# Performance work log

Hardware: AMD Instinct MI355X
Metric: run time of the kernel (lower is better)

Reference implementation:

```python
import jax, jax.numpy as jnp
import numpy as np

N_WAY, K_SHOT = 5, 1
N_CLASSES = 64
D = 8


def _conv(x, w, b):
    y = jax.lax.conv_general_dilated(x, w, (2, 2), 'SAME',
                                     dimension_numbers=('NCHW', 'OIHW', 'NCHW'))
    return jax.nn.relu(y + b[None, :, None, None])


def setup_inputs() -> dict:
    key = jax.random.key(0)
    ks = jax.random.split(key, 12)
    b, s_sup, q, h, w = 4, N_WAY * K_SHOT, 1, 64, 64
    rnd = lambda k, shape: jax.random.normal(k, shape, jnp.float32) * 0.05
    return {
        'support_x': jax.random.normal(ks[0], (b, s_sup, 3, h, w), jnp.float32),
        'support_y': jax.random.randint(ks[1], (b, s_sup), 0, N_CLASSES),
        'query_x': jax.random.normal(ks[2], (b, q, 3, h, w), jnp.float32),
        'query_y': jax.random.randint(ks[3], (b, q), 0, N_CLASSES),
        'k1': rnd(ks[4], (32, 3, 3, 3)), 'bc1': jnp.zeros((32,), jnp.float32),
        'k2': rnd(ks[5], (48, 32, 3, 3)), 'bc2': jnp.zeros((48,), jnp.float32),
        'k3': rnd(ks[6], (64, 48, 3, 3)), 'bc3': jnp.zeros((64,), jnp.float32),
        'Wlog': rnd(ks[7], (64, N_CLASSES)), 'blog': jnp.zeros((N_CLASSES,), jnp.float32),
        'Wg1': rnd(ks[8], (132, 128)), 'bg1': jnp.zeros((128,), jnp.float32),
        'Wg2': rnd(ks[9], (128, 64)), 'bg2': jnp.zeros((64,), jnp.float32),
        'Wf1': rnd(ks[10], (64, 16)), 'bf1': jnp.zeros((16,), jnp.float32),
        'Wf2': rnd(ks[11], (16, 1)), 'bf2': jnp.zeros((1,), jnp.float32),
    }


def reference(support_x, support_y, query_x, query_y,
              k1, bc1, k2, bc2, k3, bc3, Wlog, blog,
              Wg1, bg1, Wg2, bg2, Wf1, bf1, Wf2, bf2):
    x = jnp.concatenate([support_x, query_x], axis=1)       # [b, s, 3, h, w]
    label = jnp.concatenate([support_y, query_y], axis=1)   # [b, s]
    b, s = label.shape
    h, w = x.shape[-2:]

    feat = x.reshape(b * s, 3, h, w)
    feat = _conv(feat, k1, bc1)
    feat = _conv(feat, k2, bc2)
    feat = _conv(feat, k3, bc3)                              # [b*s, c, D, D]
    c = feat.shape[1]
    logits = feat.mean(axis=(2, 3)) @ Wlog + blog            # [b*s, n_classes]

    # --- append normalized (i/d, j/d) coord channels ---
    ii = jnp.arange(D, dtype=feat.dtype) / D
    coord = jnp.stack([jnp.broadcast_to(ii[:, None], (D, D)),
                       jnp.broadcast_to(ii[None, :], (D, D))])        # [2, D, D]
    feat = feat.reshape(b, s, c, D, D)
    feat = jnp.concatenate([feat, jnp.broadcast_to(coord, (b, s, 2, D, D))], axis=2)
    c2 = c + 2
    m = D * D
    a = feat.reshape(b, s, c2, m).transpose(0, 1, 3, 2)      # [b, s, m, c2]

    # --- relation network g over all (set-pair, position-pair) combos ---
    # original: g(concat(x_i, x_j)) where x_i = x[b, j, :, q], x_j = x[b, i, :, p]
    # split first linear: concat @ Wg1 = x_i @ Wg1[:c2] + x_j @ Wg1[c2:]
    W1a, W1b = Wg1[:c2], Wg1[c2:]
    u = a @ W1a                                              # [b, s_j, m_q, 128]
    v = a @ W1b + bg1                                        # [b, s_i, m_p, 128]
    # hdd[b,i,j,q,p] = relu(u[b,j,q] + v[b,i,p])  -> [b, s, s, m, m, 128]
    hdd = jax.nn.relu(u[:, None, :, :, None, :] + v[:, :, None, None, :, :])
    g = jax.nn.relu(hdd @ Wg2 + bg2)                         # [b, s, s, m, m, 64]
    x_f = g.sum(axis=(3, 4))                                 # [b, s, s, 64]
    score = jax.nn.sigmoid(jax.nn.relu(x_f @ Wf1 + bf1) @ Wf2 + bf2)  # [b, s, s, 1]

    # --- losses ---
    logp = jax.nn.log_softmax(logits, axis=-1)
    lab = label.reshape(-1)
    cls_loss = -jnp.take_along_axis(logp, lab[:, None], axis=1).mean()

    y = (label[:, :, None] == label[:, None, :])[..., None].astype(score.dtype)
    P = score[..., 0]                                        # [b, s, s]
    Pt = P.transpose(0, 2, 1)
    sym, anti = 0.5 * (P + Pt), 0.5 * (P - Pt)
    sym_n = jnp.sqrt((sym ** 2).sum(axis=(1, 2)))            # Frobenius per batch
    anti_n = jnp.sqrt((anti ** 2).sum(axis=(1, 2)))
    sym_loss = ((sym_n - anti_n) / (sym_n + anti_n)).mean()
    euc_loss = ((score - y) ** 2).mean()
    rn_loss = euc_loss - 0.1 * sym_loss
    return (cls_loss, rn_loss, sym_loss)
```

## Files before the change

### kernel.cpp

```cpp
#include <hip/hip_runtime.h>

typedef _Float16 f16x8 __attribute__((ext_vector_type(8)));
typedef float f32x4 __attribute__((ext_vector_type(4)));

__global__ void conv1_k(const float* __restrict__ sx, const float* __restrict__ qx,
                        const float* __restrict__ w, const float* __restrict__ bias,
                        float* __restrict__ out,
                        const float* __restrict__ Wg2, _Float16* __restrict__ W2h) {
    if (blockIdx.x == 768) {
        for (int s = 0; s < 4; s++) {
            int slot = threadIdx.x + 256*s;
            int tile = slot >> 6, lane = slot & 63;
            int kt = tile >> 2, nt = tile & 3;
            int quad = lane >> 4, col = lane & 15;
            f16x8 t;
            #pragma unroll
            for (int jj = 0; jj < 8; jj++)
                t[jj] = (_Float16)Wg2[(kt*32 + quad*8 + jj)*64 + nt*16 + col];
            *(f16x8*)&W2h[slot*8] = t;
        }
        return;
    }
    int n  = blockIdx.x >> 5;
    int oc = blockIdx.x & 31;
    int bi = n / 6, si = n % 6;
    const float* inp = (si < 5) ? sx + (size_t)((bi*5+si)*3)*4096
                                : qx + (size_t)(bi*3)*4096;
    __shared__ float wl[27];
    __shared__ float bl;
    if (threadIdx.x < 27) wl[threadIdx.x] = w[oc*27 + threadIdx.x];
    if (threadIdx.x == 0) bl = bias[oc];
    __syncthreads();
    for (int idx = threadIdx.x; idx < 1024; idx += 256) {
        int oy = idx >> 5, ox = idx & 31;
        float acc = bl;
        #pragma unroll
        for (int ic = 0; ic < 3; ic++) {
            const float* ip = inp + ic*4096;
            #pragma unroll
            for (int dy = 0; dy < 3; dy++) {
                int iy = 2*oy + dy;
                if (iy >= 64) continue;
                #pragma unroll
                for (int dx = 0; dx < 3; dx++) {
                    int ix = 2*ox + dx;
                    if (ix >= 64) continue;
                    acc += ip[iy*64+ix] * wl[ic*9 + dy*3 + dx];
                }
            }
        }
        out[(size_t)(n*32+oc)*1024 + idx] = fmaxf(acc, 0.f);
    }
}

__global__ void conv2_k(const float* __restrict__ in, const float* __restrict__ w,
                        const float* __restrict__ bias, float* __restrict__ out) {
    int n   = blockIdx.x / 12;
    int ocg = blockIdx.x % 12;
    __shared__ float wl[4*32*9];
    for (int e = threadIdx.x; e < 1152; e += 256) wl[e] = w[ocg*4*288 + e];
    __syncthreads();
    int oy = threadIdx.x >> 4, ox = threadIdx.x & 15;
    float a0 = bias[ocg*4+0], a1 = bias[ocg*4+1], a2 = bias[ocg*4+2], a3 = bias[ocg*4+3];
    const float* ib = in + (size_t)n*32*1024;
    for (int ic = 0; ic < 32; ic++) {
        const float* ip = ib + ic*1024;
        float tap[9];
        #pragma unroll
        for (int dy = 0; dy < 3; dy++)
            #pragma unroll
            for (int dx = 0; dx < 3; dx++) {
                int iy = 2*oy+dy, ix = 2*ox+dx;
                tap[dy*3+dx] = (iy < 32 && ix < 32) ? ip[iy*32+ix] : 0.f;
            }
        #pragma unroll
        for (int t = 0; t < 9; t++) {
            a0 += tap[t]*wl[0*288 + ic*9 + t];
            a1 += tap[t]*wl[1*288 + ic*9 + t];
            a2 += tap[t]*wl[2*288 + ic*9 + t];
            a3 += tap[t]*wl[3*288 + ic*9 + t];
        }
    }
    size_t ob = (size_t)(n*48 + ocg*4)*256 + threadIdx.x;
    out[ob        ] = fmaxf(a0, 0.f);
    out[ob + 256  ] = fmaxf(a1, 0.f);
    out[ob + 512  ] = fmaxf(a2, 0.f);
    out[ob + 768  ] = fmaxf(a3, 0.f);
}

__global__ void conv3_k(const float* __restrict__ in, const float* __restrict__ w,
                        const float* __restrict__ bias, float* __restrict__ out,
                        float* __restrict__ mf) {
    int n   = blockIdx.x >> 3;
    int ocg = blockIdx.x & 7;
    __shared__ float wl[8*48*9];
    for (int e = threadIdx.x; e < 3456; e += 256) wl[e] = w[ocg*8*432 + e];
    __syncthreads();
    int pix = threadIdx.x & 63, osub = threadIdx.x >> 6;
    int oy = pix >> 3, ox = pix & 7;
    int ol0 = osub*2;
    float a0 = bias[ocg*8 + ol0], a1 = bias[ocg*8 + ol0 + 1];
    const float* ib = in + (size_t)n*48*256;
    for (int ic = 0; ic < 48; ic++) {
        const float* ip = ib + ic*256;
        float tap[9];
        #pragma unroll
        for (int dy = 0; dy < 3; dy++)
            #pragma unroll
            for (int dx = 0; dx < 3; dx++) {
                int iy = 2*oy+dy, ix = 2*ox+dx;
                tap[dy*3+dx] = (iy < 16 && ix < 16) ? ip[iy*16+ix] : 0.f;
            }
        #pragma unroll
        for (int t = 0; t < 9; t++) {
            a0 += tap[t]*wl[ ol0   *432 + ic*9 + t];
            a1 += tap[t]*wl[(ol0+1)*432 + ic*9 + t];
        }
    }
    float r0 = fmaxf(a0, 0.f), r1 = fmaxf(a1, 0.f);
    out[(size_t)(n*64 + ocg*8 + ol0  )*64 + pix] = r0;
    out[(size_t)(n*64 + ocg*8 + ol0+1)*64 + pix] = r1;
    #pragma unroll
    for (int off = 32; off >= 1; off >>= 1) {
        r0 += __shfl_xor(r0, off, 64);
        r1 += __shfl_xor(r1, off, 64);
    }
    if (pix == 0) {
        mf[n*64 + ocg*8 + ol0    ] = r0 * (1.f/64.f);
        mf[n*64 + ocg*8 + ol0 + 1] = r1 * (1.f/64.f);
    }
}

__global__ void uvcls_k(const float* __restrict__ feat3, const float* __restrict__ Wg1,
                        const float* __restrict__ bg1, _Float16* __restrict__ u,
                        _Float16* __restrict__ v,
                        const float* __restrict__ mf, const int* __restrict__ sy,
                        const int* __restrict__ qy, const float* __restrict__ Wlog,
                        const float* __restrict__ blog, float* __restrict__ rv) {
    int tid = threadIdx.x;
    if (blockIdx.x >= 384) {
        int n = blockIdx.x - 384;
        if (tid >= 64) return;
        int lane = tid;
        float s = blog[lane];
        for (int c = 0; c < 64; c++) s += mf[n*64 + c] * Wlog[c*64 + lane];
        float mx = s;
        #pragma unroll
        for (int off = 32; off >= 1; off >>= 1) mx = fmaxf(mx, __shfl_xor(mx, off, 64));
        float p = __expf(s - mx);
        float se = p;
        #pragma unroll
        for (int off = 32; off >= 1; off >>= 1) se += __shfl_xor(se, off, 64);
        int bi = n/6, si = n%6;
        int lab = (si < 5) ? sy[bi*5+si] : qy[bi];
        float s_lab = __shfl(s, lab, 64);
        if (lane == 0) rv[n] = -(s_lab - mx - __logf(se));
        return;
    }
    int bs = blockIdx.x >> 4;
    int pg = blockIdx.x & 15;
    __shared__ float a4[4][66];
    for (int e = tid; e < 264; e += 128) {
        int pl = e / 66, c = e % 66;
        int p = pg*4 + pl;
        float vv;
        if (c < 64)       vv = feat3[(size_t)(bs*64 + c)*64 + p];
        else if (c == 64) vv = (float)(p >> 3) * 0.125f;
        else              vv = (float)(p & 7) * 0.125f;
        a4[pl][c] = vv;
    }
    __syncthreads();
    float us[4] = {0.f,0.f,0.f,0.f};
    float bg = bg1[tid];
    float vs[4] = {bg,bg,bg,bg};
    for (int c = 0; c < 66; c++) {
        float wa = Wg1[c*128 + tid];
        float wb = Wg1[(66+c)*128 + tid];
        #pragma unroll
        for (int pl = 0; pl < 4; pl++) {
            us[pl] += a4[pl][c]*wa;
            vs[pl] += a4[pl][c]*wb;
        }
    }
    #pragma unroll
    for (int pl = 0; pl < 4; pl++) {
        int p = pg*4 + pl;
        u[(size_t)(bs*64+p)*128 + tid] = (_Float16)us[pl];
        v[(size_t)(bs*64+p)*128 + tid] = (_Float16)vs[pl];
    }
}

__global__ void __launch_bounds__(256) rel_k(
        const _Float16* __restrict__ U, const _Float16* __restrict__ V,
        const _Float16* __restrict__ W2h, const float* __restrict__ bg2,
        float* __restrict__ xfpart) {
    __shared__ __align__(16) _Float16 Vsh[16*128];
    __shared__ float xfred[4][64];

    int bx = blockIdx.x;
    int cb = bx >> 2, qc = bx & 3;
    int b = cb / 36, rem = cb % 36;
    int j = rem / 6, i = rem % 6;
    int tid  = threadIdx.x;
    int wv   = tid >> 6, lane = tid & 63;
    int col  = lane & 15, quad = lane >> 4;

    const _Float16* ub = U + (size_t)(b*6 + i)*8192;
    const _Float16* vb = V + (size_t)(b*6 + j)*8192 + qc*16*128;

    *(f16x8*)&Vsh[tid*8] = *(const f16x8*)&vb[tid*8];

    f16x8 uf[4];
    {
        const _Float16* up = ub + (wv*16 + col)*128 + quad*8;
        #pragma unroll
        for (int kt = 0; kt < 4; kt++) uf[kt] = *(const f16x8*)&up[kt*32];
    }
    f16x8 bf[4][4];
    #pragma unroll
    for (int kt = 0; kt < 4; kt++)
        #pragma unroll
        for (int nt = 0; nt < 4; nt++)
            bf[kt][nt] = *(const f16x8*)&W2h[(size_t)(((kt*4+nt)*64) + lane)*8];
    float bgv[4];
    #pragma unroll
    for (int nt = 0; nt < 4; nt++) bgv[nt] = bg2[nt*16 + col];

    __syncthreads();

    float sums[4] = {0.f,0.f,0.f,0.f};
    for (int q = 0; q < 16; q++) {
        const _Float16* vp = &Vsh[q*128 + quad*8];
        f32x4 acc[4];
        #pragma unroll
        for (int nt = 0; nt < 4; nt++)
            acc[nt] = (f32x4){bgv[nt], bgv[nt], bgv[nt], bgv[nt]};
        #pragma unroll
        for (int kt = 0; kt < 4; kt++) {
            f16x8 vf = *(const f16x8*)&vp[kt*32];
            f16x8 af = uf[kt] + vf;
            af = __builtin_elementwise_max(af, (f16x8){0,0,0,0,0,0,0,0});
            #pragma unroll
            for (int nt = 0; nt < 4; nt++)
                acc[nt] = __builtin_amdgcn_mfma_f32_16x16x32_f16(af, bf[kt][nt], acc[nt], 0, 0, 0);
        }
        #pragma unroll
        for (int nt = 0; nt < 4; nt++)
            #pragma unroll
            for (int rr = 0; rr < 4; rr++)
                sums[nt] += fmaxf(acc[nt][rr], 0.f);
    }

    #pragma unroll
    for (int nt = 0; nt < 4; nt++) {
        sums[nt] += __shfl_xor(sums[nt], 16, 64);
        sums[nt] += __shfl_xor(sums[nt], 32, 64);
    }
    if (lane < 16) {
        #pragma unroll
        for (int nt = 0; nt < 4; nt++) xfred[wv][nt*16 + lane] = sums[nt];
    }
    __syncthreads();
    if (tid < 64)
        xfpart[(size_t)bx*64 + tid] = xfred[0][tid] + xfred[1][tid] + xfred[2][tid] + xfred[3][tid];
}

__global__ void loss_k(const float* __restrict__ xfp, const float* __restrict__ rv,
                       const int* __restrict__ sy, const int* __restrict__ qy,
                       const float* __restrict__ Wf1, const float* __restrict__ bf1,
                       const float* __restrict__ Wf2, const float* __restrict__ bf2,
                       float* __restrict__ out) {
    __shared__ float Wf1sh[1024];
    __shared__ float wf2sh[16];
    __shared__ float bf1sh[16];
    __shared__ float Pm[144];
    __shared__ int lab[24];
    __shared__ float red[256];
    __shared__ float ratio[4];
    int tid = threadIdx.x;
    for (int e = tid; e < 1024; e += 256) Wf1sh[e] = Wf1[e];
    if (tid < 16) { wf2sh[tid] = Wf2[tid]; bf1sh[tid] = bf1[tid]; }
    if (tid < 24) { int bi = tid/6, si = tid%6; lab[tid] = (si < 5) ? sy[bi*5+si] : qy[bi]; }
    __syncthreads();
    if (tid < 144) {
        float hid[16];
        #pragma unroll
        for (int h = 0; h < 16; h++) hid[h] = bf1sh[h];
        const float* xb = xfp + (size_t)tid*4*64;
        for (int n = 0; n < 64; n++) {
            float x = xb[n] + xb[64+n] + xb[128+n] + xb[192+n];
            #pragma unroll
            for (int h = 0; h < 16; h++) hid[h] += x * Wf1sh[n*16 + h];
        }
        float sc = bf2[0];
        #pragma unroll
        for (int h = 0; h < 16; h++) sc += fmaxf(hid[h], 0.f) * wf2sh[h];
        Pm[tid] = 1.f/(1.f + __expf(-sc));
    }
    __syncthreads();
    float e = 0.f;
    if (tid < 144) {
        int b = tid/36, r = tid%36, jj = r/6, ii = r%6;
        float y = (lab[b*6+jj] == lab[b*6+ii]) ? 1.f : 0.f;
        float d = Pm[tid] - y;
        e = d*d;
    }
    red[tid] = e;
    __syncthreads();
    for (int s = 128; s > 0; s >>= 1) {
        if (tid < s) red[tid] += red[tid+s];
        __syncthreads();
    }
    if (tid < 4) {
        float s2 = 0.f, a2 = 0.f;
        for (int jj = 0; jj < 6; jj++)
            for (int ii = 0; ii < 6; ii++) {
                float pa = Pm[tid*36 + jj*6 + ii], pb = Pm[tid*36 + ii*6 + jj];
                float sm = 0.5f*(pa+pb), an = 0.5f*(pa-pb);
                s2 += sm*sm; a2 += an*an;
            }
        float sn = sqrtf(s2), anq = sqrtf(a2);
        ratio[tid] = (sn - anq)/(sn + anq);
    }
    __syncthreads();
    if (tid == 0) {
        float sl = 0.25f*(ratio[0]+ratio[1]+ratio[2]+ratio[3]);
        float euc = red[0] * (1.f/144.f);
        float cs = 0.f;
        for (int k = 0; k < 24; k++) cs += rv[k];
        out[0] = cs * (1.f/24.f);
        out[1] = euc - 0.1f*sl;
        out[2] = sl;
    }
}

extern "C" void kernel_launch(void* const* d_in, const int* in_sizes, int n_in,
                              void* d_out, int out_size, void* d_ws, size_t ws_size,
                              hipStream_t stream) {
    const float* sx   = (const float*)d_in[0];
    const int*   sy   = (const int*)  d_in[1];
    const float* qx   = (const float*)d_in[2];
    const int*   qy   = (const int*)  d_in[3];
    const float* k1   = (const float*)d_in[4];
    const float* bc1  = (const float*)d_in[5];
    const float* k2   = (const float*)d_in[6];
    const float* bc2  = (const float*)d_in[7];
    const float* k3   = (const float*)d_in[8];
    const float* bc3  = (const float*)d_in[9];
    const float* Wlog = (const float*)d_in[10];
    const float* blog = (const float*)d_in[11];
    const float* Wg1  = (const float*)d_in[12];
    const float* bg1  = (const float*)d_in[13];
    const float* Wg2  = (const float*)d_in[14];
    const float* bg2  = (const float*)d_in[15];
    const float* Wf1  = (const float*)d_in[16];
    const float* bf1  = (const float*)d_in[17];
    const float* Wf2  = (const float*)d_in[18];
    const float* bf2  = (const float*)d_in[19];

    float* ws    = (float*)d_ws;
    float* feat1 = ws;
    float* feat2 = feat1 + 786432;
    float* feat3 = feat2 + 294912;
    float* mf    = feat3 + 98304;
    float* rv    = mf    + 1536;
    float* xfp   = rv    + 32;
    _Float16* u16 = (_Float16*)(xfp + 36864);
    _Float16* v16 = u16 + 196608;
    _Float16* W2h = v16 + 196608;
    float* out   = (float*)d_out;

    conv1_k <<<769,    256, 0, stream>>>(sx, qx, k1, bc1, feat1, Wg2, W2h);
    conv2_k <<<24*12,  256, 0, stream>>>(feat1, k2, bc2, feat2);
    conv3_k <<<24*8,   256, 0, stream>>>(feat2, k3, bc3, feat3, mf);
    uvcls_k <<<408,    128, 0, stream>>>(feat3, Wg1, bg1, u16, v16,
                                         mf, sy, qy, Wlog, blog, rv);
    rel_k   <<<576,    256, 0, stream>>>(u16, v16, W2h, bg2, xfp);
    loss_k  <<<1,      256, 0, stream>>>(xfp, rv, sy, qy, Wf1, bf1, Wf2, bf2, out);
}
```

Measured before the change: 189.7 us.

## Fuse all stages into one persistent kernel with software grid barriers

Replaces the six separate kernel launches with one persistent mega-kernel sized to occupancy. Stages are separated by an atomic-counter global barrier, and blocks loop over each stage's work chunks. The goal is to remove per-launch overhead and the idle gaps between stages. The uv projection now packs two pixel groups per 256-thread block, and the relation partial sums are stored transposed so the loss stage can read them as vector loads. The barrier depends on every block being resident at once. The counter is never reset but grows monotonically across calls, which may eventually risk wraparound.

```diff
diff --git a/kernel.cpp b/kernel.cpp
--- a/kernel.cpp
+++ b/kernel.cpp
@@ -3,378 +3,395 @@
 typedef _Float16 f16x8 __attribute__((ext_vector_type(8)));
 typedef float f32x4 __attribute__((ext_vector_type(4)));
 
-__global__ void conv1_k(const float* __restrict__ sx, const float* __restrict__ qx,
-                        const float* __restrict__ w, const float* __restrict__ bias,
-                        float* __restrict__ out,
-                        const float* __restrict__ Wg2, _Float16* __restrict__ W2h) {
-    if (blockIdx.x == 768) {
-        for (int s = 0; s < 4; s++) {
-            int slot = threadIdx.x + 256*s;
-            int tile = slot >> 6, lane = slot & 63;
-            int kt = tile >> 2, nt = tile & 3;
-            int quad = lane >> 4, col = lane & 15;
-            f16x8 t;
-            #pragma unroll
-            for (int jj = 0; jj < 8; jj++)
-                t[jj] = (_Float16)Wg2[(kt*32 + quad*8 + jj)*64 + nt*16 + col];
-            *(f16x8*)&W2h[slot*8] = t;
-        }
-        return;
-    }
-    int n  = blockIdx.x >> 5;
-    int oc = blockIdx.x & 31;
-    int bi = n / 6, si = n % 6;
-    const float* inp = (si < 5) ? sx + (size_t)((bi*5+si)*3)*4096
-                                : qx + (size_t)(bi*3)*4096;
-    __shared__ float wl[27];
-    __shared__ float bl;
-    if (threadIdx.x < 27) wl[threadIdx.x] = w[oc*27 + threadIdx.x];
-    if (threadIdx.x == 0) bl = bias[oc];
+__device__ unsigned g_bar_count = 0;
+
+struct MegaP {
+    const float* sx; const int* sy; const float* qx; const int* qy;
+    const float* k1; const float* bc1; const float* k2; const float* bc2;
+    const float* k3; const float* bc3; const float* Wlog; const float* blog;
+    const float* Wg1; const float* bg1; const float* Wg2; const float* bg2;
+    const float* Wf1; const float* bf1; const float* Wf2; const float* bf2;
+    float* feat1; float* feat2; float* feat3; float* mf; float* rv; float* xfpT;
+    _Float16* u16; _Float16* v16; _Float16* W2h; float* out;
+};
+
+__device__ __forceinline__ void gbar() {
     __syncthreads();
-    for (int idx = threadIdx.x; idx < 1024; idx += 256) {
-        int oy = idx >> 5, ox = idx & 31;
-        float acc = bl;
+    if (threadIdx.x == 0) {
+        __threadfence();
+        unsigned nb = gridDim.x;
+        unsigned my = __hip_atomic_fetch_add(&g_bar_count, 1u, __ATOMIC_ACQ_REL,
+                                             __HIP_MEMORY_SCOPE_AGENT) + 1u;
+        unsigned tgt = ((my + nb - 1u) / nb) * nb;
+        while (__hip_atomic_load(&g_bar_count, __ATOMIC_ACQUIRE,
+                                 __HIP_MEMORY_SCOPE_AGENT) < tgt)
+            __builtin_amdgcn_s_sleep(2);
+    }
+    __syncthreads();
+    __threadfence();
+}
+
+__global__ void __launch_bounds__(256, 2) mega_k(MegaP P) {
+    __shared__ __align__(16) float smem[3456];
+    const int tid = threadIdx.x;
+    const unsigned gsz = gridDim.x;
+
+    for (unsigned ch = blockIdx.x; ch < 769; ch += gsz) {
+        if (ch == 768) {
+            for (int s = 0; s < 4; s++) {
+                int slot = tid + 256*s;
+                int tile = slot >> 6, lane = slot & 63;
+                int kt = tile >> 2, nt = tile & 3;
+                int quad = lane >> 4, col = lane & 15;
+                f16x8 t;
+                #pragma unroll
+                for (int jj = 0; jj < 8; jj++)
+                    t[jj] = (_Float16)P.Wg2[(kt*32 + quad*8 + jj)*64 + nt*16 + col];
+                *(f16x8*)&P.W2h[slot*8] = t;
+            }
+        } else {
+            int n  = (int)ch >> 5;
+            int oc = (int)ch & 31;
+            int bi = n / 6, si = n % 6;
+            const float* inp = (si < 5) ? P.sx + (size_t)((bi*5+si)*3)*4096
+                                        : P.qx + (size_t)(bi*3)*4096;
+            __syncthreads();
+            if (tid < 27) smem[tid] = P.k1[oc*27 + tid];
+            if (tid == 31) smem[27] = P.bc1[oc];
+            __syncthreads();
+            float bl = smem[27];
+            for (int idx = tid; idx < 1024; idx += 256) {
+                int oy = idx >> 5, ox = idx & 31;
+                float acc = bl;
+                #pragma unroll
+                for (int ic = 0; ic < 3; ic++) {
+                    const float* ip = inp + ic*4096;
+                    #pragma unroll
+                    for (int dy = 0; dy < 3; dy++) {
+                        int iy = 2*oy + dy;
+                        if (iy >= 64) continue;
+                        #pragma unroll
+                        for (int dx = 0; dx < 3; dx++) {
+                            int ix = 2*ox + dx;
+                            if (ix >= 64) continue;
+                            acc += ip[iy*64+ix] * smem[ic*9 + dy*3 + dx];
+                        }
+                    }
+                }
+                P.feat1[(size_t)(n*32+oc)*1024 + idx] = fmaxf(acc, 0.f);
+            }
+        }
+    }
+    gbar();
+
+    for (unsigned ch = blockIdx.x; ch < 288; ch += gsz) {
+        int n   = (int)ch / 12;
+        int ocg = (int)ch % 12;
+        __syncthreads();
+        for (int e = tid; e < 1152; e += 256) smem[e] = P.k2[ocg*1152 + e];
+        __syncthreads();
+        int oy = tid >> 4, ox = tid & 15;
+        float a0 = P.bc2[ocg*4+0], a1 = P.bc2[ocg*4+1];
+        float a2 = P.bc2[ocg*4+2], a3 = P.bc2[ocg*4+3];
+        const float* ib = P.feat1 + (size_t)n*32*1024;
+        for (int ic = 0; ic < 32; ic++) {
+            const float* ip = ib + ic*1024;
+            float tap[9];
+            #pragma unroll
+            for (int dy = 0; dy < 3; dy++)
+                #pragma unroll
+                for (int dx = 0; dx < 3; dx++) {
+                    int iy = 2*oy+dy, ix = 2*ox+dx;
+                    tap[dy*3+dx] = (iy < 32 && ix < 32) ? ip[iy*32+ix] : 0.f;
+                }
+            #pragma unroll
+            for (int t = 0; t < 9; t++) {
+                a0 += tap[t]*smem[0*288 + ic*9 + t];
+                a1 += tap[t]*smem[1*288 + ic*9 + t];
+                a2 += tap[t]*smem[2*288 + ic*9 + t];
+                a3 += tap[t]*smem[3*288 + ic*9 + t];
+            }
+        }
+        size_t ob = (size_t)(n*48 + ocg*4)*256 + tid;
+        P.feat2[ob        ] = fmaxf(a0, 0.f);
+        P.feat2[ob + 256  ] = fmaxf(a1, 0.f);
+        P.feat2[ob + 512  ] = fmaxf(a2, 0.f);
+        P.feat2[ob + 768  ] = fmaxf(a3, 0.f);
+    }
+    gbar();
+
+    for (unsigned ch = blockIdx.x; ch < 192; ch += gsz) {
+        int n   = (int)ch >> 3;
+        int ocg = (int)ch & 7;
+        __syncthreads();
+        for (int e = tid; e < 3456; e += 256) smem[e] = P.k3[ocg*3456 + e];
+        __syncthreads();
+        int pix = tid & 63, osub = tid >> 6;
+        int oy = pix >> 3, ox = pix & 7;
+        int ol0 = osub*2;
+        float a0 = P.bc3[ocg*8 + ol0], a1 = P.bc3[ocg*8 + ol0 + 1];
+        const float* ib = P.feat2 + (size_t)n*48*256;
+        for (int ic = 0; ic < 48; ic++) {
+            const float* ip = ib + ic*256;
+            float tap[9];
+            #pragma unroll
+            for (int dy = 0; dy < 3; dy++)
+                #pragma unroll
+                for (int dx = 0; dx < 3; dx++) {
+                    int iy = 2*oy+dy, ix = 2*ox+dx;
+                    tap[dy*3+dx] = (iy < 16 && ix < 16) ? ip[iy*16+ix] : 0.f;
+                }
+            #pragma unroll
+            for (int t = 0; t < 9; t++) {
+                a0 += tap[t]*smem[ ol0   *432 + ic*9 + t];
+                a1 += tap[t]*smem[(ol0+1)*432 + ic*9 + t];
+            }
+        }
+        float r0 = fmaxf(a0, 0.f), r1 = fmaxf(a1, 0.f);
+        P.feat3[(size_t)(n*64 + ocg*8 + ol0  )*64 + pix] = r0;
+        P.feat3[(size_t)(n*64 + ocg*8 + ol0+1)*64 + pix] = r1;
         #pragma unroll
-        for (int ic = 0; ic < 3; ic++) {
-            const float* ip = inp + ic*4096;
-            #pragma unroll
-            for (int dy = 0; dy < 3; dy++) {
-                int iy = 2*oy + dy;
-                if (iy >= 64) continue;
-                #pragma unroll
-                for (int dx = 0; dx < 3; dx++) {
-                    int ix = 2*ox + dx;
-                    if (ix >= 64) continue;
-                    acc += ip[iy*64+ix] * wl[ic*9 + dy*3 + dx];
-                }
-            }
-        }
-        out[(size_t)(n*32+oc)*1024 + idx] = fmaxf(acc, 0.f);
-    }
-}
-
-__global__ void conv2_k(const float* __restrict__ in, const float* __restrict__ w,
-                        const float* __restrict__ bias, float* __restrict__ out) {
-    int n   = blockIdx.x / 12;
-    int ocg = blockIdx.x % 12;
-    __shared__ float wl[4*32*9];
-    for (int e = threadIdx.x; e < 1152; e += 256) wl[e] = w[ocg*4*288 + e];
-    __syncthreads();
-    int oy = threadIdx.x >> 4, ox = threadIdx.x & 15;
-    float a0 = bias[ocg*4+0], a1 = bias[ocg*4+1], a2 = bias[ocg*4+2], a3 = bias[ocg*4+3];
-    const float* ib = in + (size_t)n*32*1024;
-    for (int ic = 0; ic < 32; ic++) {
-        const float* ip = ib + ic*1024;
-        float tap[9];
+        for (int off = 32; off >= 1; off >>= 1) {
+            r0 += __shfl_xor(r0, off, 64);
+            r1 += __shfl_xor(r1, off, 64);
+        }
+        if (pix == 0) {
+            P.mf[n*64 + ocg*8 + ol0    ] = r0 * (1.f/64.f);
+            P.mf[n*64 + ocg*8 + ol0 + 1] = r1 * (1.f/64.f);
+        }
+    }
+    gbar();
+
+    for (unsigned ch = blockIdx.x; ch < 216; ch += gsz) {
+        if (ch < 192) {
+            int bs = (int)ch >> 3, pp = (int)ch & 7;
+            int half = tid >> 7, t = tid & 127;
+            int pg = pp*2 + half;
+            float (*a4)[66] = ((float(*)[66])smem) + half*4;
+            __syncthreads();
+            for (int e = t; e < 264; e += 128) {
+                int pl = e / 66, c = e % 66;
+                int p = pg*4 + pl;
+                float vv;
+                if (c < 64)       vv = P.feat3[(size_t)(bs*64 + c)*64 + p];
+                else if (c == 64) vv = (float)(p >> 3) * 0.125f;
+                else              vv = (float)(p & 7) * 0.125f;
+                a4[pl][c] = vv;
+            }
+            __syncthreads();
+            float us[4] = {0.f,0.f,0.f,0.f};
+            float bg = P.bg1[t];
+            float vs[4] = {bg,bg,bg,bg};
+            for (int c = 0; c < 66; c++) {
+                float wa = P.Wg1[c*128 + t];
+                float wb = P.Wg1[(66+c)*128 + t];
+                #pragma unroll
+                for (int pl = 0; pl < 4; pl++) {
+                    us[pl] += a4[pl][c]*wa;
+                    vs[pl] += a4[pl][c]*wb;
+                }
+            }
+            #pragma unroll
+            for (int pl = 0; pl < 4; pl++) {
+                int p = pg*4 + pl;
+                P.u16[(size_t)(bs*64+p)*128 + t] = (_Float16)us[pl];
+                P.v16[(size_t)(bs*64+p)*128 + t] = (_Float16)vs[pl];
+            }
+        } else {
+            int n = (int)ch - 192;
+            if (tid < 64) {
+                float s = P.blog[tid];
+                for (int c = 0; c < 64; c++) s += P.mf[n*64 + c] * P.Wlog[c*64 + tid];
+                float mx = s;
+                #pragma unroll
+                for (int off = 32; off >= 1; off >>= 1) mx = fmaxf(mx, __shfl_xor(mx, off, 64));
+                float px = __expf(s - mx);
+                float se = px;
+                #pragma unroll
+                for (int off = 32; off >= 1; off >>= 1) se += __shfl_xor(se, off, 64);
+                int bi = n/6, si = n%6;
+                int lab = (si < 5) ? P.sy[bi*5+si] : P.qy[bi];
+                float s_lab = __shfl(s, lab, 64);
+                if (tid == 0) P.rv[n] = -(s_lab - mx - __logf(se));
+            }
+        }
+    }
+    gbar();
+
+    {
+        int wv = tid >> 6, lane = tid & 63;
+        int col = lane & 15, quad = lane >> 4;
+        f16x8 bf[4][4];
         #pragma unroll
-        for (int dy = 0; dy < 3; dy++)
-            #pragma unroll
-            for (int dx = 0; dx < 3; dx++) {
-                int iy = 2*oy+dy, ix = 2*ox+dx;
-                tap[dy*3+dx] = (iy < 32 && ix < 32) ? ip[iy*32+ix] : 0.f;
-            }
+        for (int kt = 0; kt < 4; kt++)
+            #pragma unroll
+            for (int nt = 0; nt < 4; nt++)
+                bf[kt][nt] = *(const f16x8*)&P.W2h[(size_t)(((kt*4+nt)*64) + lane)*8];
+        float bgv[4];
         #pragma unroll
-        for (int t = 0; t < 9; t++) {
-            a0 += tap[t]*wl[0*288 + ic*9 + t];
-            a1 += tap[t]*wl[1*288 + ic*9 + t];
-            a2 += tap[t]*wl[2*288 + ic*9 + t];
-            a3 += tap[t]*wl[3*288 + ic*9 + t];
-        }
-    }
-    size_t ob = (size_t)(n*48 + ocg*4)*256 + threadIdx.x;
-    out[ob        ] = fmaxf(a0, 0.f);
-    out[ob + 256  ] = fmaxf(a1, 0.f);
-    out[ob + 512  ] = fmaxf(a2, 0.f);
-    out[ob + 768  ] = fmaxf(a3, 0.f);
-}
-
-__global__ void conv3_k(const float* __restrict__ in, const float* __restrict__ w,
-                        const float* __restrict__ bias, float* __restrict__ out,
-                        float* __restrict__ mf) {
-    int n   = blockIdx.x >> 3;
-    int ocg = blockIdx.x & 7;
-    __shared__ float wl[8*48*9];
-    for (int e = threadIdx.x; e < 3456; e += 256) wl[e] = w[ocg*8*432 + e];
-    __syncthreads();
-    int pix = threadIdx.x & 63, osub = threadIdx.x >> 6;
-    int oy = pix >> 3, ox = pix & 7;
-    int ol0 = osub*2;
-    float a0 = bias[ocg*8 + ol0], a1 = bias[ocg*8 + ol0 + 1];
-    const float* ib = in + (size_t)n*48*256;
-    for (int ic = 0; ic < 48; ic++) {
-        const float* ip = ib + ic*256;
-        float tap[9];
-        #pragma unroll
-        for (int dy = 0; dy < 3; dy++)
-            #pragma unroll
-            for (int dx = 0; dx < 3; dx++) {
-                int iy = 2*oy+dy, ix = 2*ox+dx;
-                tap[dy*3+dx] = (iy < 16 && ix < 16) ? ip[iy*16+ix] : 0.f;
-            }
-        #pragma unroll
-        for (int t = 0; t < 9; t++) {
-            a0 += tap[t]*wl[ ol0   *432 + ic*9 + t];
-            a1 += tap[t]*wl[(ol0+1)*432 + ic*9 + t];
-        }
-    }
-    float r0 = fmaxf(a0, 0.f), r1 = fmaxf(a1, 0.f);
-    out[(size_t)(n*64 + ocg*8 + ol0  )*64 + pix] = r0;
-    out[(size_t)(n*64 + ocg*8 + ol0+1)*64 + pix] = r1;
-    #pragma unroll
-    for (int off = 32; off >= 1; off >>= 1) {
-        r0 += __shfl_xor(r0, off, 64);
-        r1 += __shfl_xor(r1, off, 64);
-    }
-    if (pix == 0) {
-        mf[n*64 + ocg*8 + ol0    ] = r0 * (1.f/64.f);
-        mf[n*64 + ocg*8 + ol0 + 1] = r1 * (1.f/64.f);
-    }
-}
-
-__global__ void uvcls_k(const float* __restrict__ feat3, const float* __restrict__ Wg1,
-                        const float* __restrict__ bg1, _Float16* __restrict__ u,
-                        _Float16* __restrict__ v,
-                        const float* __restrict__ mf, const int* __restrict__ sy,
-                        const int* __restrict__ qy, const float* __restrict__ Wlog,
-                        const float* __restrict__ blog, float* __restrict__ rv) {
-    int tid = threadIdx.x;
-    if (blockIdx.x >= 384) {
-        int n = blockIdx.x - 384;
-        if (tid >= 64) return;
-        int lane = tid;
-        float s = blog[lane];
-        for (int c = 0; c < 64; c++) s += mf[n*64 + c] * Wlog[c*64 + lane];
-        float mx = s;
-        #pragma unroll
-        for (int off = 32; off >= 1; off >>= 1) mx = fmaxf(mx, __shfl_xor(mx, off, 64));
-        float p = __expf(s - mx);
-        float se = p;
-        #pragma unroll
-        for (int off = 32; off >= 1; off >>= 1) se += __shfl_xor(se, off, 64);
-        int bi = n/6, si = n%6;
-        int lab = (si < 5) ? sy[bi*5+si] : qy[bi];
-        float s_lab = __shfl(s, lab, 64);
-        if (lane == 0) rv[n] = -(s_lab - mx - __logf(se));
-        return;
-    }
-    int bs = blockIdx.x >> 4;
-    int pg = blockIdx.x & 15;
-    __shared__ float a4[4][66];
-    for (int e = tid; e < 264; e += 128) {
-        int pl = e / 66, c = e % 66;
-        int p = pg*4 + pl;
-        float vv;
-        if (c < 64)       vv = feat3[(size_t)(bs*64 + c)*64 + p];
-        else if (c == 64) vv = (float)(p >> 3) * 0.125f;
-        else              vv = (float)(p & 7) * 0.125f;
-        a4[pl][c] = vv;
-    }
-    __syncthreads();
-    float us[4] = {0.f,0.f,0.f,0.f};
-    float bg = bg1[tid];
-    float vs[4] = {bg,bg,bg,bg};
-    for (int c = 0; c < 66; c++) {
-        float wa = Wg1[c*128 + tid];
-        float wb = Wg1[(66+c)*128 + tid];
-        #pragma unroll
-        for (int pl = 0; pl < 4; pl++) {
-            us[pl] += a4[pl][c]*wa;
-            vs[pl] += a4[pl][c]*wb;
-        }
-    }
-    #pragma unroll
-    for (int pl = 0; pl < 4; pl++) {
-        int p = pg*4 + pl;
-        u[(size_t)(bs*64+p)*128 + tid] = (_Float16)us[pl];
-        v[(size_t)(bs*64+p)*128 + tid] = (_Float16)vs[pl];
-    }
-}
-
-__global__ void __launch_bounds__(256) rel_k(
-        const _Float16* __restrict__ U, const _Float16* __restrict__ V,
-        const _Float16* __restrict__ W2h, const float* __restrict__ bg2,
-        float* __restrict__ xfpart) {
-    __shared__ __align__(16) _Float16 Vsh[16*128];
-    __shared__ float xfred[4][64];
-
-    int bx = blockIdx.x;
-    int cb = bx >> 2, qc = bx & 3;
-    int b = cb / 36, rem = cb % 36;
-    int j = rem / 6, i = rem % 6;
-    int tid  = threadIdx.x;
-    int wv   = tid >> 6, lane = tid & 63;
-    int col  = lane & 15, quad = lane >> 4;
-
-    const _Float16* ub = U + (size_t)(b*6 + i)*8192;
-    const _Float16* vb = V + (size_t)(b*6 + j)*8192 + qc*16*128;
-
-    *(f16x8*)&Vsh[tid*8] = *(const f16x8*)&vb[tid*8];
-
-    f16x8 uf[4];
-    {
-        const _Float16* up = ub + (wv*16 + col)*128 + quad*8;
-        #pragma unroll
-        for (int kt = 0; kt < 4; kt++) uf[kt] = *(const f16x8*)&up[kt*32];
-    }
-    f16x8 bf[4][4];
-    #pragma unroll
-    for (int kt = 0; kt < 4; kt++)
-        #pragma unroll
-        for (int nt = 0; nt < 4; nt++)
-            bf[kt][nt] = *(const f16x8*)&W2h[(size_t)(((kt*4+nt)*64) + lane)*8];
-    float bgv[4];
-    #pragma unroll
-    for (int nt = 0; nt < 4; nt++) bgv[nt] = bg2[nt*16 + col];
-
-    __syncthreads();
-
-    float sums[4] = {0.f,0.f,0.f,0.f};
-    for (int q = 0; q < 16; q++) {
-        const _Float16* vp = &Vsh[q*128 + quad*8];
-        f32x4 acc[4];
-        #pragma unroll
-        for (int nt = 0; nt < 4; nt++)
-            acc[nt] = (f32x4){bgv[nt], bgv[nt], bgv[nt], bgv[nt]};
-        #pragma unroll
-        for (int kt = 0; kt < 4; kt++) {
-            f16x8 vf = *(const f16x8*)&vp[kt*32];
-            f16x8 af = uf[kt] + vf;
-            af = __builtin_elementwise_max(af, (f16x8){0,0,0,0,0,0,0,0});
-            #pragma unroll
-            for (int nt = 0; nt < 4; nt++)
-                acc[nt] = __builtin_amdgcn_mfma_f32_16x16x32_f16(af, bf[kt][nt], acc[nt], 0, 0, 0);
-        }
-        #pragma unroll
-        for (int nt = 0; nt < 4; nt++)
-            #pragma unroll
-            for (int rr = 0; rr < 4; rr++)
-                sums[nt] += fmaxf(acc[nt][rr], 0.f);
-    }
-
-    #pragma unroll
-    for (int nt = 0; nt < 4; nt++) {
-        sums[nt] += __shfl_xor(sums[nt], 16, 64);
-        sums[nt] += __shfl_xor(sums[nt], 32, 64);
-    }
-    if (lane < 16) {
-        #pragma unroll
-        for (int nt = 0; nt < 4; nt++) xfred[wv][nt*16 + lane] = sums[nt];
-    }
-    __syncthreads();
-    if (tid < 64)
-        xfpart[(size_t)bx*64 + tid] = xfred[0][tid] + xfred[1][tid] + xfred[2][tid] + xfred[3][tid];
-}
-
-__global__ void loss_k(const float* __restrict__ xfp, const float* __restrict__ rv,
-                       const int* __restrict__ sy, const int* __restrict__ qy,
-                       const float* __restrict__ Wf1, const float* __restrict__ bf1,
-                       const float* __restrict__ Wf2, const float* __restrict__ bf2,
-                       float* __restrict__ out) {
-    __shared__ float Wf1sh[1024];
-    __shared__ float wf2sh[16];
-    __shared__ float bf1sh[16];
-    __shared__ float Pm[144];
-    __shared__ int lab[24];
-    __shared__ float red[256];
-    __shared__ float ratio[4];
-    int tid = threadIdx.x;
-    for (int e = tid; e < 1024; e += 256) Wf1sh[e] = Wf1[e];
-    if (tid < 16) { wf2sh[tid] = Wf2[tid]; bf1sh[tid] = bf1[tid]; }
-    if (tid < 24) { int bi = tid/6, si = tid%6; lab[tid] = (si < 5) ? sy[bi*5+si] : qy[bi]; }
-    __syncthreads();
-    if (tid < 144) {
-        float hid[16];
-        #pragma unroll
-        for (int h = 0; h < 16; h++) hid[h] = bf1sh[h];
-        const float* xb = xfp + (size_t)tid*4*64;
-        for (int n = 0; n < 64; n++) {
-            float x = xb[n] + xb[64+n] + xb[128+n] + xb[192+n];
-            #pragma unroll
-            for (int h = 0; h < 16; h++) hid[h] += x * Wf1sh[n*16 + h];
-        }
-        float sc = bf2[0];
-        #pragma unroll
-        for (int h = 0; h < 16; h++) sc += fmaxf(hid[h], 0.f) * wf2sh[h];
-        Pm[tid] = 1.f/(1.f + __expf(-sc));
-    }
-    __syncthreads();
-    float e = 0.f;
-    if (tid < 144) {
-        int b = tid/36, r = tid%36, jj = r/6, ii = r%6;
-        float y = (lab[b*6+jj] == lab[b*6+ii]) ? 1.f : 0.f;
-        float d = Pm[tid] - y;
-        e = d*d;
-    }
-    red[tid] = e;
-    __syncthreads();
-    for (int s = 128; s > 0; s >>= 1) {
-        if (tid < s) red[tid] += red[tid+s];
-        __syncthreads();
-    }
-    if (tid < 4) {
-        float s2 = 0.f, a2 = 0.f;
-        for (int jj = 0; jj < 6; jj++)
-            for (int ii = 0; ii < 6; ii++) {
-                float pa = Pm[tid*36 + jj*6 + ii], pb = Pm[tid*36 + ii*6 + jj];
-                float sm = 0.5f*(pa+pb), an = 0.5f*(pa-pb);
-                s2 += sm*sm; a2 += an*an;
-            }
-        float sn = sqrtf(s2), anq = sqrtf(a2);
-        ratio[tid] = (sn - anq)/(sn + anq);
-    }
-    __syncthreads();
-    if (tid == 0) {
-        float sl = 0.25f*(ratio[0]+ratio[1]+ratio[2]+ratio[3]);
-        float euc = red[0] * (1.f/144.f);
-        float cs = 0.f;
-        for (int k = 0; k < 24; k++) cs += rv[k];
-        out[0] = cs * (1.f/24.f);
-        out[1] = euc - 0.1f*sl;
-        out[2] = sl;
+        for (int nt = 0; nt < 4; nt++) bgv[nt] = P.bg2[nt*16 + col];
+        _Float16* Vsh  = (_Float16*)smem;
+        float*    xfred = smem + 1024;
+
+        for (unsigned ch = blockIdx.x; ch < 576; ch += gsz) {
+            int cb = (int)ch >> 2, qc = (int)ch & 3;
+            int b = cb / 36, rem = cb % 36;
+            int j = rem / 6, i = rem % 6;
+            const _Float16* ub = P.u16 + (size_t)(b*6 + i)*8192;
+            const _Float16* vb = P.v16 + (size_t)(b*6 + j)*8192 + qc*2048;
+            __syncthreads();
+            *(f16x8*)&Vsh[tid*8] = *(const f16x8*)&vb[tid*8];
+            f16x8 uf[4];
+            {
+                const _Float16* up = ub + (wv*16 + col)*128 + quad*8;
+                #pragma unroll
+                for (int kt = 0; kt < 4; kt++) uf[kt] = *(const f16x8*)&up[kt*32];
+            }
+            __syncthreads();
+            float sums[4] = {0.f,0.f,0.f,0.f};
+            for (int q = 0; q < 16; q++) {
+                const _Float16* vp = &Vsh[q*128 + quad*8];
+                f32x4 acc[4];
+                #pragma unroll
+                for (int nt = 0; nt < 4; nt++)
+                    acc[nt] = (f32x4){bgv[nt], bgv[nt], bgv[nt], bgv[nt]};
+                #pragma unroll
+                for (int kt = 0; kt < 4; kt++) {
+                    f16x8 vf = *(const f16x8*)&vp[kt*32];
+                    f16x8 af = uf[kt] + vf;
+                    af = __builtin_elementwise_max(af, (f16x8){0,0,0,0,0,0,0,0});
+                    #pragma unroll
+                    for (int nt = 0; nt < 4; nt++)
+                        acc[nt] = __builtin_amdgcn_mfma_f32_16x16x32_f16(af, bf[kt][nt], acc[nt], 0, 0, 0);
+                }
+                #pragma unroll
+                for (int nt = 0; nt < 4; nt++)
+                    #pragma unroll
+                    for (int rr = 0; rr < 4; rr++)
+                        sums[nt] += fmaxf(acc[nt][rr], 0.f);
+            }
+            #pragma unroll
+            for (int nt = 0; nt < 4; nt++) {
+                sums[nt] += __shfl_xor(sums[nt], 16, 64);
+                sums[nt] += __shfl_xor(sums[nt], 32, 64);
+            }
+            if (lane < 16) {
+                #pragma unroll
+                for (int nt = 0; nt < 4; nt++) xfred[wv*64 + nt*16 + lane] = sums[nt];
+            }
+            __syncthreads();
+            if (tid < 64)
+                P.xfpT[(size_t)tid*576 + ch] =
+                    xfred[tid] + xfred[64+tid] + xfred[128+tid] + xfred[192+tid];
+        }
+    }
+    gbar();
+
+    if (blockIdx.x == 0) {
+        float* Wf1sh = smem;
+        float* wf2sh = smem + 1024;
+        float* bf1sh = smem + 1040;
+        float* Pmm   = smem + 1056;
+        int*   lab   = (int*)(smem + 1200);
+        float* red   = smem + 1232;
+        float* ratio = smem + 1488;
+        for (int e = tid; e < 1024; e += 256) Wf1sh[e] = P.Wf1[e];
+        if (tid < 16) { wf2sh[tid] = P.Wf2[tid]; bf1sh[tid] = P.bf1[tid]; }
+        if (tid < 24) { int bi = tid/6, si = tid%6; lab[tid] = (si < 5) ? P.sy[bi*5+si] : P.qy[bi]; }
+        __syncthreads();
+        if (tid < 144) {
+            float hid[16];
+            #pragma unroll
+            for (int h = 0; h < 16; h++) hid[h] = bf1sh[h];
+            for (int n = 0; n < 64; n++) {
+                f32x4 vv = *(const f32x4*)&P.xfpT[(size_t)n*576 + tid*4];
+                float x = vv[0] + vv[1] + vv[2] + vv[3];
+                #pragma unroll
+                for (int h = 0; h < 16; h++) hid[h] += x * Wf1sh[n*16 + h];
+            }
+            float sc = P.bf2[0];
+            #pragma unroll
+            for (int h = 0; h < 16; h++) sc += fmaxf(hid[h], 0.f) * wf2sh[h];
+            Pmm[tid] = 1.f/(1.f + __expf(-sc));
+        }
+        __syncthreads();
+        float e = 0.f;
+        if (tid < 144) {
+            int b = tid/36, r = tid%36, jj = r/6, ii = r%6;
+            float y = (lab[b*6+jj] == lab[b*6+ii]) ? 1.f : 0.f;
+            float d = Pmm[tid] - y;
+            e = d*d;
+        }
+        red[tid] = e;
+        __syncthreads();
+        for (int s = 128; s > 0; s >>= 1) {
+            if (tid < s) red[tid] += red[tid+s];
+            __syncthreads();
+        }
+        if (tid < 4) {
+            float s2 = 0.f, a2 = 0.f;
+            for (int jj = 0; jj < 6; jj++)
+                for (int ii = 0; ii < 6; ii++) {
+                    float pa = Pmm[tid*36 + jj*6 + ii], pb = Pmm[tid*36 + ii*6 + jj];
+                    float sm = 0.5f*(pa+pb), an = 0.5f*(pa-pb);
+                    s2 += sm*sm; a2 += an*an;
+                }
+            float sn = sqrtf(s2), anq = sqrtf(a2);
+            ratio[tid] = (sn - anq)/(sn + anq);
+        }
+        __syncthreads();
+        if (tid == 0) {
+            float sl = 0.25f*(ratio[0]+ratio[1]+ratio[2]+ratio[3]);
+            float euc = red[0] * (1.f/144.f);
+            float cs = 0.f;
+            for (int k = 0; k < 24; k++) cs += P.rv[k];
+            P.out[0] = cs * (1.f/24.f);
+            P.out[1] = euc - 0.1f*sl;
+            P.out[2] = sl;
+        }
     }
 }
 
 extern "C" void kernel_launch(void* const* d_in, const int* in_sizes, int n_in,
                               void* d_out, int out_size, void* d_ws, size_t ws_size,
                               hipStream_t stream) {
-    const float* sx   = (const float*)d_in[0];
-    const int*   sy   = (const int*)  d_in[1];
-    const float* qx   = (const float*)d_in[2];
-    const int*   qy   = (const int*)  d_in[3];
-    const float* k1   = (const float*)d_in[4];
-    const float* bc1  = (const float*)d_in[5];
-    const float* k2   = (const float*)d_in[6];
-    const float* bc2  = (const float*)d_in[7];
-    const float* k3   = (const float*)d_in[8];
-    const float* bc3  = (const float*)d_in[9];
-    const float* Wlog = (const float*)d_in[10];
-    const float* blog = (const float*)d_in[11];
-    const float* Wg1  = (const float*)d_in[12];
-    const float* bg1  = (const float*)d_in[13];
-    const float* Wg2  = (const float*)d_in[14];
-    const float* bg2  = (const float*)d_in[15];
-    const float* Wf1  = (const float*)d_in[16];
-    const float* bf1  = (const float*)d_in[17];
-    const float* Wf2  = (const float*)d_in[18];
-    const float* bf2  = (const float*)d_in[19];
-
     float* ws    = (float*)d_ws;
     float* feat1 = ws;
     float* feat2 = feat1 + 786432;
     float* feat3 = feat2 + 294912;
     float* mf    = feat3 + 98304;
     float* rv    = mf    + 1536;
-    float* xfp   = rv    + 32;
-    _Float16* u16 = (_Float16*)(xfp + 36864);
+    float* xfpT  = rv    + 32;
+    _Float16* u16 = (_Float16*)(xfpT + 36864);
     _Float16* v16 = u16 + 196608;
     _Float16* W2h = v16 + 196608;
-    float* out   = (float*)d_out;
-
-    conv1_k <<<769,    256, 0, stream>>>(sx, qx, k1, bc1, feat1, Wg2, W2h);
-    conv2_k <<<24*12,  256, 0, stream>>>(feat1, k2, bc2, feat2);
-    conv3_k <<<24*8,   256, 0, stream>>>(feat2, k3, bc3, feat3, mf);
-    uvcls_k <<<408,    128, 0, stream>>>(feat3, Wg1, bg1, u16, v16,
-                                         mf, sy, qy, Wlog, blog, rv);
-    rel_k   <<<576,    256, 0, stream>>>(u16, v16, W2h, bg2, xfp);
-    loss_k  <<<1,      256, 0, stream>>>(xfp, rv, sy, qy, Wf1, bf1, Wf2, bf2, out);
+
+    MegaP P;
+    P.sx = (const float*)d_in[0];  P.sy  = (const int*)d_in[1];
+    P.qx = (const float*)d_in[2];  P.qy  = (const int*)d_in[3];
+    P.k1 = (const float*)d_in[4];  P.bc1 = (const float*)d_in[5];
+    P.k2 = (const float*)d_in[6];  P.bc2 = (const float*)d_in[7];
+    P.k3 = (const float*)d_in[8];  P.bc3 = (const float*)d_in[9];
+    P.Wlog = (const float*)d_in[10]; P.blog = (const float*)d_in[11];
+    P.Wg1  = (const float*)d_in[12]; P.bg1  = (const float*)d_in[13];
+    P.Wg2  = (const float*)d_in[14]; P.bg2  = (const float*)d_in[15];
+    P.Wf1  = (const float*)d_in[16]; P.bf1  = (const float*)d_in[17];
+    P.Wf2  = (const float*)d_in[18]; P.bf2  = (const float*)d_in[19];
+    P.feat1 = feat1; P.feat2 = feat2; P.feat3 = feat3; P.mf = mf; P.rv = rv;
+    P.xfpT = xfpT; P.u16 = u16; P.v16 = v16; P.W2h = W2h; P.out = (float*)d_out;
+
+    static int grid = 0;
+    if (grid == 0) {
+        int nb = 0;
+        if (hipOccupancyMaxActiveBlocksPerMultiprocessor(&nb, mega_k, 256, 0) != hipSuccess || nb < 1)
+            nb = 1;
+        int dev = 0;
+        hipGetDevice(&dev);
+        hipDeviceProp_t prop;
+        int ncu = (hipGetDeviceProperties(&prop, dev) == hipSuccess) ? prop.multiProcessorCount : 0;
+        if (ncu < 1) ncu = 64;
+        long g = (long)nb * (long)ncu;
+        grid = (int)(g < 576 ? g : 576);
+    }
+    hipLaunchKernelGGL(mega_k, dim3(grid), dim3(256), 0, stream, P);
 }
```

Result: slower. 454.7 us (+139.7%).

## Remap block indices for XCD locality and stage conv2/conv3 inputs in LDS

Applied to the files above, without the earlier changes.

Block indices across conv1, conv2, conv3, uvcls and rel kernels are remapped so that blockIdx & 7 selects the sample or batch, aiming to place blocks that share input data on the same XCD's L2 under round-robin dispatch. conv2 and conv3 now stage each input channel plane in padded shared memory with a triple buffer and register prefetch two channels ahead, replacing strided global tap reads. This adds a __syncthreads per input channel and more LDS per block, which may reduce occupancy and add barrier cost.

```diff
diff --git a/kernel.cpp b/kernel.cpp
--- a/kernel.cpp
+++ b/kernel.cpp
@@ -2,6 +2,7 @@
 
 typedef _Float16 f16x8 __attribute__((ext_vector_type(8)));
 typedef float f32x4 __attribute__((ext_vector_type(4)));
+
 
 __global__ void conv1_k(const float* __restrict__ sx, const float* __restrict__ qx,
                         const float* __restrict__ w, const float* __restrict__ bias,
@@ -21,8 +22,9 @@
         }
         return;
     }
-    int n  = blockIdx.x >> 5;
-    int oc = blockIdx.x & 31;
+    int r8 = blockIdx.x & 7, q = blockIdx.x >> 3;
+    int n  = (q >> 5)*8 + r8;
+    int oc = q & 31;
     int bi = n / 6, si = n % 6;
     const float* inp = (si < 5) ? sx + (size_t)((bi*5+si)*3)*4096
                                 : qx + (size_t)(bi*3)*4096;
@@ -55,23 +57,36 @@
 
 __global__ void conv2_k(const float* __restrict__ in, const float* __restrict__ w,
                         const float* __restrict__ bias, float* __restrict__ out) {
-    int n   = blockIdx.x / 12;
-    int ocg = blockIdx.x % 12;
-    __shared__ float wl[4*32*9];
-    for (int e = threadIdx.x; e < 1152; e += 256) wl[e] = w[ocg*4*288 + e];
-    __syncthreads();
-    int oy = threadIdx.x >> 4, ox = threadIdx.x & 15;
-    float a0 = bias[ocg*4+0], a1 = bias[ocg*4+1], a2 = bias[ocg*4+2], a3 = bias[ocg*4+3];
+    int r8 = blockIdx.x & 7, q = blockIdx.x >> 3;
+    int n   = (q / 12)*8 + r8;
+    int ocg = q % 12;
+    __shared__ float wl[1152];
+    __shared__ float pin[3][33*32];
+    const int tid = threadIdx.x;
+    for (int e = tid; e < 1152; e += 256) wl[e] = w[ocg*1152 + e];
     const float* ib = in + (size_t)n*32*1024;
+    int srow = (tid*4) >> 5, scol = (tid*4) & 31;
+    {
+        f32x4 t0 = *(const f32x4*)&ib[tid*4];
+        float* d = &pin[0][srow*33 + scol];
+        d[0]=t0[0]; d[1]=t0[1]; d[2]=t0[2]; d[3]=t0[3];
+    }
+    f32x4 t1 = *(const f32x4*)&ib[1024 + tid*4];
+    __syncthreads();
+    int oy = tid >> 4, ox = tid & 15;
+    float a0 = bias[ocg*4+0], a1 = bias[ocg*4+1];
+    float a2 = bias[ocg*4+2], a3 = bias[ocg*4+3];
     for (int ic = 0; ic < 32; ic++) {
-        const float* ip = ib + ic*1024;
+        f32x4 t2 = t1;
+        if (ic + 2 < 32) t2 = *(const f32x4*)&ib[(size_t)(ic+2)*1024 + tid*4];
+        const float* pp = pin[ic % 3];
         float tap[9];
         #pragma unroll
         for (int dy = 0; dy < 3; dy++)
             #pragma unroll
             for (int dx = 0; dx < 3; dx++) {
                 int iy = 2*oy+dy, ix = 2*ox+dx;
-                tap[dy*3+dx] = (iy < 32 && ix < 32) ? ip[iy*32+ix] : 0.f;
+                tap[dy*3+dx] = (iy < 32 && ix < 32) ? pp[iy*33 + ix] : 0.f;
             }
         #pragma unroll
         for (int t = 0; t < 9; t++) {
@@ -80,8 +95,14 @@
             a2 += tap[t]*wl[2*288 + ic*9 + t];
             a3 += tap[t]*wl[3*288 + ic*9 + t];
         }
-    }
-    size_t ob = (size_t)(n*48 + ocg*4)*256 + threadIdx.x;
+        if (ic + 1 < 32) {
+            float* d = &pin[(ic+1) % 3][srow*33 + scol];
+            d[0]=t1[0]; d[1]=t1[1]; d[2]=t1[2]; d[3]=t1[3];
+        }
+        t1 = t2;
+        __syncthreads();
+    }
+    size_t ob = (size_t)(n*48 + ocg*4)*256 + tid;
     out[ob        ] = fmaxf(a0, 0.f);
     out[ob + 256  ] = fmaxf(a1, 0.f);
     out[ob + 512  ] = fmaxf(a2, 0.f);
@@ -91,31 +112,42 @@
 __global__ void conv3_k(const float* __restrict__ in, const float* __restrict__ w,
                         const float* __restrict__ bias, float* __restrict__ out,
                         float* __restrict__ mf) {
-    int n   = blockIdx.x >> 3;
-    int ocg = blockIdx.x & 7;
-    __shared__ float wl[8*48*9];
-    for (int e = threadIdx.x; e < 3456; e += 256) wl[e] = w[ocg*8*432 + e];
-    __syncthreads();
-    int pix = threadIdx.x & 63, osub = threadIdx.x >> 6;
+    int r8 = blockIdx.x & 7, q = blockIdx.x >> 3;
+    int n   = (q >> 3)*8 + r8;
+    int ocg = q & 7;
+    __shared__ float wl[3456];
+    __shared__ float pin[3][17*16];
+    const int tid = threadIdx.x;
+    for (int e = tid; e < 3456; e += 256) wl[e] = w[ocg*3456 + e];
+    const float* ib = in + (size_t)n*48*256;
+    int srow = tid >> 4, scol = tid & 15;
+    pin[0][srow*17 + scol] = ib[tid];
+    float t1 = ib[256 + tid];
+    __syncthreads();
+    int pix = tid & 63, osub = tid >> 6;
     int oy = pix >> 3, ox = pix & 7;
     int ol0 = osub*2;
     float a0 = bias[ocg*8 + ol0], a1 = bias[ocg*8 + ol0 + 1];
-    const float* ib = in + (size_t)n*48*256;
     for (int ic = 0; ic < 48; ic++) {
-        const float* ip = ib + ic*256;
+        float t2 = t1;
+        if (ic + 2 < 48) t2 = ib[(size_t)(ic+2)*256 + tid];
+        const float* pp = pin[ic % 3];
         float tap[9];
         #pragma unroll
         for (int dy = 0; dy < 3; dy++)
             #pragma unroll
             for (int dx = 0; dx < 3; dx++) {
                 int iy = 2*oy+dy, ix = 2*ox+dx;
-                tap[dy*3+dx] = (iy < 16 && ix < 16) ? ip[iy*16+ix] : 0.f;
+                tap[dy*3+dx] = (iy < 16 && ix < 16) ? pp[iy*17 + ix] : 0.f;
             }
         #pragma unroll
         for (int t = 0; t < 9; t++) {
             a0 += tap[t]*wl[ ol0   *432 + ic*9 + t];
             a1 += tap[t]*wl[(ol0+1)*432 + ic*9 + t];
         }
+        if (ic + 1 < 48) pin[(ic+1) % 3][srow*17 + scol] = t1;
+        t1 = t2;
+        __syncthreads();
     }
     float r0 = fmaxf(a0, 0.f), r1 = fmaxf(a1, 0.f);
     out[(size_t)(n*64 + ocg*8 + ol0  )*64 + pix] = r0;
@@ -157,8 +189,9 @@
         if (lane == 0) rv[n] = -(s_lab - mx - __logf(se));
         return;
     }
-    int bs = blockIdx.x >> 4;
-    int pg = blockIdx.x & 15;
+    int r8 = blockIdx.x & 7, q = blockIdx.x >> 3;
+    int bs = (q >> 4)*8 + r8;
+    int pg = q & 15;
     __shared__ float a4[4][66];
     for (int e = tid; e < 264; e += 128) {
         int pl = e / 66, c = e % 66;
@@ -197,10 +230,11 @@
     __shared__ __align__(16) _Float16 Vsh[16*128];
     __shared__ float xfred[4][64];
 
-    int bx = blockIdx.x;
-    int cb = bx >> 2, qc = bx & 3;
-    int b = cb / 36, rem = cb % 36;
-    int j = rem / 6, i = rem % 6;
+    int r8 = blockIdx.x & 7, qq = blockIdx.x >> 3;
+    int b = r8 >> 1;
+    int m = (qq << 1) | (r8 & 1);
+    int cb = m >> 2, qc = m & 3;
+    int j = cb / 6, i = cb % 6;
     int tid  = threadIdx.x;
     int wv   = tid >> 6, lane = tid & 63;
     int col  = lane & 15, quad = lane >> 4;
@@ -262,7 +296,8 @@
     }
     __syncthreads();
     if (tid < 64)
-        xfpart[(size_t)bx*64 + tid] = xfred[0][tid] + xfred[1][tid] + xfred[2][tid] + xfred[3][tid];
+        xfpart[(size_t)(b*144 + m)*64 + tid] =
+            xfred[0][tid] + xfred[1][tid] + xfred[2][tid] + xfred[3][tid];
 }
 
 __global__ void loss_k(const float* __restrict__ xfp, const float* __restrict__ rv,
```

New measurement: 178.5 us. 5.9% less time.
